# Kernel tuning notes

Measured on AMD Instinct MI355X. Metric: run time of the kernel, lower is better.

Reference implementation:

```python
import jax, jax.numpy as jnp
import numpy as np

SEQ_LEN, KEY_DIM, VAL_DIM, NUM_FEATURES, BATCH = 2048, 512, 512, 1024, 8


def setup_inputs() -> dict:
    key = jax.random.key(0)
    ks = jax.random.split(key, 7)
    x = jax.random.normal(ks[0], (BATCH, SEQ_LEN, NUM_FEATURES), dtype=jnp.float32)
    s = 1.0 / np.sqrt(NUM_FEATURES)
    Wq = jax.random.normal(ks[1], (NUM_FEATURES, KEY_DIM), dtype=jnp.float32) * s
    bq = jnp.zeros((KEY_DIM,), dtype=jnp.float32)
    Wk = jax.random.normal(ks[2], (NUM_FEATURES, KEY_DIM), dtype=jnp.float32) * s
    bk = jnp.zeros((KEY_DIM,), dtype=jnp.float32)
    Wv = jax.random.normal(ks[3], (NUM_FEATURES, VAL_DIM), dtype=jnp.float32) * s
    bv = jnp.zeros((VAL_DIM,), dtype=jnp.float32)
    return {"x": x, "Wq": Wq, "bq": bq, "Wk": Wk, "bk": bk, "Wv": Wv, "bv": bv}


def reference(x, Wq, bq, Wk, bk, Wv, bv):
    # x: [B, S, F]
    S = x.shape[1]
    q = x @ Wq + bq                      # [B, S, K]
    k = x @ Wk + bk                      # [B, S, K]
    v = x @ Wv + bv                      # [B, S, V]
    logits = jnp.einsum('bqd,bkd->bqk', q, k) / jnp.sqrt(jnp.float32(KEY_DIM))
    # additive causal mask: -inf above diagonal
    causal = jnp.tril(jnp.ones((S, S), dtype=bool))
    logits = jnp.where(causal, logits, -jnp.inf)
    probs = jax.nn.softmax(logits, axis=-1)
    read = jnp.einsum('bqk,bkv->bqv', probs, v)  # [B, S, V]
    return jnp.concatenate([x, read], axis=-1)   # [B, S, F+V]
```

## Files before the change

### kernel.cpp

```cpp
#include <hip/hip_runtime.h>

#define BB 8
#define SS 2048
#define FF 1024
#define DD 512

typedef __attribute__((ext_vector_type(4))) float f32x4;
typedef __attribute__((ext_vector_type(8))) short s16x8;
typedef __attribute__((ext_vector_type(4))) short s16x4;

__device__ __forceinline__ unsigned short f2bf(float f) {
  unsigned int u = __builtin_bit_cast(unsigned int, f);
  unsigned int r = ((u >> 16) & 1u) + 0x7fffu;
  return (unsigned short)((u + r) >> 16);
}

__device__ __forceinline__ void async16(const void* g, void* l) {
  __builtin_amdgcn_global_load_lds((const __attribute__((address_space(1))) void*)g,
                                   (__attribute__((address_space(3))) void*)l, 16, 0, 0);
}

__global__ __launch_bounds__(256) void convert_x(const float* __restrict__ x,
                                                 float* __restrict__ out,
                                                 unsigned short* __restrict__ xb) {
  size_t idx = ((size_t)blockIdx.x * 256 + threadIdx.x) * 4;
  f32x4 v = *(const f32x4*)(x + idx);
  size_t row = idx >> 10;
  size_t col = idx & 1023;
  *(f32x4*)(out + row * 1536 + col) = v;
  s16x4 h;
  h[0] = (short)f2bf(v[0]); h[1] = (short)f2bf(v[1]);
  h[2] = (short)f2bf(v[2]); h[3] = (short)f2bf(v[3]);
  *(s16x4*)(xb + idx) = h;
}

__global__ __launch_bounds__(256) void prep_w(const float* __restrict__ Wq,
                                              const float* __restrict__ Wk,
                                              const float* __restrict__ Wv,
                                              unsigned short* __restrict__ wt) {
  int z = blockIdx.z;
  const float* W = (z == 0) ? Wq : ((z == 1) ? Wk : Wv);
  unsigned short* o = wt + (size_t)z * DD * FF;
  __shared__ __align__(16) float t[32][33];
  int k0 = blockIdx.x * 32, n0 = blockIdx.y * 32;
  int tid = threadIdx.x;
  int r = tid >> 3, c4 = (tid & 7) * 4;
  f32x4 v = *(const f32x4*)(W + (size_t)(k0 + r) * DD + n0 + c4);
  t[r][c4 + 0] = v[0]; t[r][c4 + 1] = v[1]; t[r][c4 + 2] = v[2]; t[r][c4 + 3] = v[3];
  __syncthreads();
  s16x4 h;
  h[0] = (short)f2bf(t[c4 + 0][r]);
  h[1] = (short)f2bf(t[c4 + 1][r]);
  h[2] = (short)f2bf(t[c4 + 2][r]);
  h[3] = (short)f2bf(t[c4 + 3][r]);
  *(s16x4*)(o + (size_t)(n0 + r) * FF + k0 + c4) = h;
}

__global__ __launch_bounds__(256, 2) void gemm_qkv(
    const unsigned short* __restrict__ xb, const unsigned short* __restrict__ wt,
    const float* __restrict__ bq, const float* __restrict__ bk, const float* __restrict__ bv,
    unsigned short* __restrict__ qo, unsigned short* __restrict__ ko,
    unsigned short* __restrict__ vto) {
  const int wsel = blockIdx.z;
  const unsigned short* W = wt + (size_t)wsel * DD * FF;
  const float* bias = (wsel == 0) ? bq : ((wsel == 1) ? bk : bv);
  const int m0 = blockIdx.x * 128, n0 = blockIdx.y * 128;

  __shared__ __align__(16) unsigned short Al[128 * 32];
  __shared__ __align__(16) unsigned short Bl[128 * 32];

  const int tid = threadIdx.x;
  const int lane = tid & 63, wv = tid >> 6;
  const int wr = wv >> 1, wc = wv & 1;
  const int l15 = lane & 15, lg = lane >> 4;

  const f32x4 fzero = {0.f, 0.f, 0.f, 0.f};
  f32x4 acc[4][4];
#pragma unroll
  for (int i = 0; i < 4; ++i)
#pragma unroll
    for (int j = 0; j < 4; ++j) acc[i][j] = fzero;

  for (int k0 = 0; k0 < FF; k0 += 32) {
#pragma unroll
    for (int is = 0; is < 2; ++is) {
      int chunk = (is * 4 + wv) * 64;
      int lin = (chunk + lane) * 8;
      int r = lin >> 5, c = lin & 31;
      async16(xb + (size_t)(m0 + r) * FF + k0 + c, (char*)Al + (size_t)chunk * 16);
      async16(W + (size_t)(n0 + r) * FF + k0 + c, (char*)Bl + (size_t)chunk * 16);
    }
    __syncthreads();
    s16x8 af[4], bf[4];
#pragma unroll
    for (int mi = 0; mi < 4; ++mi)
      af[mi] = *(const s16x8*)(&Al[(wr * 64 + mi * 16 + l15) * 32 + lg * 8]);
#pragma unroll
    for (int ni = 0; ni < 4; ++ni)
      bf[ni] = *(const s16x8*)(&Bl[(wc * 64 + ni * 16 + l15) * 32 + lg * 8]);
#pragma unroll
    for (int mi = 0; mi < 4; ++mi)
#pragma unroll
      for (int ni = 0; ni < 4; ++ni)
        acc[mi][ni] = __builtin_amdgcn_mfma_f32_16x16x32_bf16(af[mi], bf[ni], acc[mi][ni], 0, 0, 0);
    __syncthreads();
  }

  const float QS = 0.0637583894f;
#pragma unroll
  for (int ni = 0; ni < 4; ++ni) {
    int cg = n0 + wc * 64 + ni * 16 + l15;
    float bvv = bias[cg];
#pragma unroll
    for (int mi = 0; mi < 4; ++mi) {
#pragma unroll
      for (int j = 0; j < 4; ++j) {
        int rg = m0 + wr * 64 + mi * 16 + lg * 4 + j;
        float val = acc[mi][ni][j] + bvv;
        if (wsel == 0) val *= QS;
        unsigned short h = f2bf(val);
        if (wsel == 2) {
          int bb = rg >> 11, s = rg & 2047;
          vto[((size_t)(bb * DD + cg)) * SS + s] = h;
        } else {
          unsigned short* o = wsel ? ko : qo;
          o[(size_t)rg * DD + cg] = h;
        }
      }
    }
  }
}

__global__ __launch_bounds__(256, 2) void attn(const unsigned short* __restrict__ qg,
                                               const unsigned short* __restrict__ kgl,
                                               const unsigned short* __restrict__ vtg,
                                               float* __restrict__ out) {
  const int b = blockIdx.y;
  const int vhalf = blockIdx.z;
  const int qt = (vhalf == 0) ? blockIdx.x : (31 - blockIdx.x);
  const int q0 = qt * 64;

  __shared__ __align__(16) unsigned short Kl[32 * 520];
  __shared__ __align__(16) unsigned short Vl[256 * 40];
  __shared__ __align__(16) unsigned short Pl[4 * 16 * 40];

  const int tid = threadIdx.x;
  const int lane = tid & 63, w = tid >> 6;
  const int l15 = lane & 15, lg = lane >> 4;

  s16x8 qf[16];
  {
    const unsigned short* qp = qg + ((size_t)(b * SS + q0 + w * 16 + l15)) * DD + lg * 8;
#pragma unroll
    for (int kk = 0; kk < 16; ++kk) qf[kk] = *(const s16x8*)(qp + kk * 32);
  }

  const f32x4 fzero = {0.f, 0.f, 0.f, 0.f};
  f32x4 oacc[16];
#pragma unroll
  for (int n = 0; n < 16; ++n) oacc[n] = fzero;
  float mrun[4], lrun[4];
#pragma unroll
  for (int i = 0; i < 4; ++i) { mrun[i] = -__builtin_inff(); lrun[i] = 0.f; }

  const int nt = qt * 2 + 2;
  for (int t = 0; t < nt; ++t) {
    const int kv0 = t * 32;
#pragma unroll
    for (int it = 0; it < 8; ++it) {
      int lin = (it * 256 + tid) * 8;
      int r = lin >> 9, c = lin & 511;
      *(f32x4*)(&Kl[r * 520 + c]) =
          *(const f32x4*)(kgl + ((size_t)(b * SS + kv0 + r)) * DD + c);
      if (it < 4) {
        int n = lin >> 5, c2 = lin & 31;
        *(f32x4*)(&Vl[n * 40 + c2]) =
            *(const f32x4*)(vtg + ((size_t)(b * DD + vhalf * 256 + n)) * SS + kv0 + c2);
      }
    }
    __syncthreads();

    f32x4 s0 = fzero;
    f32x4 s1 = fzero;
#pragma unroll
    for (int kk = 0; kk < 16; ++kk) {
      s16x8 b0 = *(const s16x8*)(&Kl[l15 * 520 + kk * 32 + lg * 8]);
      s16x8 b1 = *(const s16x8*)(&Kl[(16 + l15) * 520 + kk * 32 + lg * 8]);
      s0 = __builtin_amdgcn_mfma_f32_16x16x32_bf16(qf[kk], b0, s0, 0, 0, 0);
      s1 = __builtin_amdgcn_mfma_f32_16x16x32_bf16(qf[kk], b1, s1, 0, 0, 0);
    }

    const int rowb = q0 + w * 16 + lg * 4;
    if (kv0 + 31 > q0 + w * 16) {
#pragma unroll
      for (int i = 0; i < 4; ++i) {
        int rg = rowb + i;
        if (kv0 + l15 > rg)      s0[i] = -__builtin_inff();
        if (kv0 + 16 + l15 > rg) s1[i] = -__builtin_inff();
      }
    }

    float corr[4];
#pragma unroll
    for (int i = 0; i < 4; ++i) {
      float tm = fmaxf(s0[i], s1[i]);
      tm = fmaxf(tm, __shfl_xor(tm, 1));
      tm = fmaxf(tm, __shfl_xor(tm, 2));
      tm = fmaxf(tm, __shfl_xor(tm, 4));
      tm = fmaxf(tm, __shfl_xor(tm, 8));
      float mo = mrun[i];
      float mn = fmaxf(mo, tm);
      mrun[i] = mn;
      float mne = fmaxf(mn, -1e30f);
      float c = __builtin_amdgcn_exp2f(fmaxf(mo, -1e30f) - mne);
      float p0 = __builtin_amdgcn_exp2f(s0[i] - mne);
      float p1 = __builtin_amdgcn_exp2f(s1[i] - mne);
      float rs = p0 + p1;
      rs += __shfl_xor(rs, 1);
      rs += __shfl_xor(rs, 2);
      rs += __shfl_xor(rs, 4);
      rs += __shfl_xor(rs, 8);
      lrun[i] = lrun[i] * c + rs;
      corr[i] = c;
      Pl[w * 640 + (lg * 4 + i) * 40 + l15] = f2bf(p0);
      Pl[w * 640 + (lg * 4 + i) * 40 + 16 + l15] = f2bf(p1);
    }

#pragma unroll
    for (int n = 0; n < 16; ++n) {
      oacc[n][0] *= corr[0]; oacc[n][1] *= corr[1];
      oacc[n][2] *= corr[2]; oacc[n][3] *= corr[3];
    }

    asm volatile("s_waitcnt lgkmcnt(0)" ::: "memory");
    s16x8 pa = *(const s16x8*)(&Pl[w * 640 + l15 * 40 + lg * 8]);
#pragma unroll
    for (int n = 0; n < 16; ++n) {
      s16x8 vb = *(const s16x8*)(&Vl[(n * 16 + l15) * 40 + lg * 8]);
      oacc[n] = __builtin_amdgcn_mfma_f32_16x16x32_bf16(pa, vb, oacc[n], 0, 0, 0);
    }
    __syncthreads();
  }

  float inv[4];
#pragma unroll
  for (int i = 0; i < 4; ++i) inv[i] = 1.0f / lrun[i];
  size_t obase = ((size_t)(b * SS + q0 + w * 16 + lg * 4)) * 1536 + 1024 + vhalf * 256;
#pragma unroll
  for (int n = 0; n < 16; ++n) {
#pragma unroll
    for (int i = 0; i < 4; ++i) {
      out[obase + (size_t)i * 1536 + n * 16 + l15] = oacc[n][i] * inv[i];
    }
  }
}

extern "C" void kernel_launch(void* const* d_in, const int* in_sizes, int n_in,
                              void* d_out, int out_size, void* d_ws, size_t ws_size,
                              hipStream_t stream) {
  (void)in_sizes; (void)n_in; (void)out_size; (void)ws_size;
  const float* x  = (const float*)d_in[0];
  const float* Wq = (const float*)d_in[1];
  const float* bq = (const float*)d_in[2];
  const float* Wk = (const float*)d_in[3];
  const float* bk = (const float*)d_in[4];
  const float* Wv = (const float*)d_in[5];
  const float* bv = (const float*)d_in[6];
  float* out = (float*)d_out;

  char* ws = (char*)d_ws;
  unsigned short* xb  = (unsigned short*)(ws);
  unsigned short* wt  = (unsigned short*)(ws + 33554432);
  unsigned short* qw  = (unsigned short*)(ws + 33554432 + 3145728);
  unsigned short* kw  = qw + (size_t)16384 * 512;
  unsigned short* vtw = kw + (size_t)16384 * 512;

  convert_x<<<16384, 256, 0, stream>>>(x, out, xb);
  prep_w<<<dim3(32, 16, 3), 256, 0, stream>>>(Wq, Wk, Wv, wt);
  gemm_qkv<<<dim3(128, 4, 3), 256, 0, stream>>>(xb, wt, bq, bk, bv, qw, kw, vtw);
  attn<<<dim3(32, 8, 2), 256, 0, stream>>>(qw, kw, vtw, out);
}
```

Before: 434.1 us.

## Use single-wave attention blocks reading K/V from global and stage V-transpose via LDS

The attention kernel is rewritten so that each 64-thread block handles 16 query rows. It loads K and V fragments directly from global memory (relying on L2/cache) instead of staging them in shared memory with block-wide barriers, and it drops the -1e30 clamping in the softmax. The grid grows to 128x8x2 with longest tiles first, to improve load balance across the causal triangle and remove syncthreads. Separately, the QKV GEMM epilogue for V now transposes through LDS and writes 16-byte vectors instead of scattered 2-byte stores. The trade-off is that K and V are no longer shared across waves in a block, so global/L2 traffic rises.

```diff
diff --git a/kernel.cpp b/kernel.cpp
--- a/kernel.cpp
+++ b/kernel.cpp
@@ -66,8 +66,9 @@
   const float* bias = (wsel == 0) ? bq : ((wsel == 1) ? bk : bv);
   const int m0 = blockIdx.x * 128, n0 = blockIdx.y * 128;
 
-  __shared__ __align__(16) unsigned short Al[128 * 32];
-  __shared__ __align__(16) unsigned short Bl[128 * 32];
+  __shared__ __align__(16) char smem[36864];
+  unsigned short* Al = (unsigned short*)smem;
+  unsigned short* Bl = (unsigned short*)(smem + 8192);
 
   const int tid = threadIdx.x;
   const int lane = tid & 63, wv = tid >> 6;
@@ -107,50 +108,66 @@
   }
 
   const float QS = 0.0637583894f;
-#pragma unroll
-  for (int ni = 0; ni < 4; ++ni) {
-    int cg = n0 + wc * 64 + ni * 16 + l15;
-    float bvv = bias[cg];
-#pragma unroll
-    for (int mi = 0; mi < 4; ++mi) {
-#pragma unroll
-      for (int j = 0; j < 4; ++j) {
-        int rg = m0 + wr * 64 + mi * 16 + lg * 4 + j;
-        float val = acc[mi][ni][j] + bvv;
-        if (wsel == 0) val *= QS;
-        unsigned short h = f2bf(val);
-        if (wsel == 2) {
-          int bb = rg >> 11, s = rg & 2047;
-          vto[((size_t)(bb * DD + cg)) * SS + s] = h;
-        } else {
-          unsigned short* o = wsel ? ko : qo;
-          o[(size_t)rg * DD + cg] = h;
+  if (wsel == 2) {
+    unsigned short* Tw = (unsigned short*)smem + (size_t)wv * 64 * 72;
+#pragma unroll
+    for (int ni = 0; ni < 4; ++ni) {
+      int cl = ni * 16 + l15;
+      float bvv = bias[n0 + wc * 64 + cl];
+#pragma unroll
+      for (int mi = 0; mi < 4; ++mi)
+#pragma unroll
+        for (int j = 0; j < 4; ++j)
+          Tw[cl * 72 + mi * 16 + lg * 4 + j] = f2bf(acc[mi][ni][j] + bvv);
+    }
+    asm volatile("s_waitcnt lgkmcnt(0)" ::: "memory");
+    const int bb = (m0 + wr * 64) >> 11;
+    const int sb = (m0 + wr * 64) & 2047;
+    const int cb = n0 + wc * 64;
+#pragma unroll
+    for (int p = 0; p < 8; ++p) {
+      int cl = p * 8 + (lane >> 3);
+      int sl = (lane & 7) * 8;
+      s16x8 vv = *(const s16x8*)(Tw + cl * 72 + sl);
+      *(s16x8*)(vto + ((size_t)(bb * DD + cb + cl)) * SS + sb + sl) = vv;
+    }
+  } else {
+    unsigned short* o = wsel ? ko : qo;
+#pragma unroll
+    for (int ni = 0; ni < 4; ++ni) {
+      int cg = n0 + wc * 64 + ni * 16 + l15;
+      float bvv = bias[cg];
+#pragma unroll
+      for (int mi = 0; mi < 4; ++mi) {
+#pragma unroll
+        for (int j = 0; j < 4; ++j) {
+          int rg = m0 + wr * 64 + mi * 16 + lg * 4 + j;
+          float val = acc[mi][ni][j] + bvv;
+          if (wsel == 0) val *= QS;
+          o[(size_t)rg * DD + cg] = f2bf(val);
         }
       }
     }
   }
 }
 
-__global__ __launch_bounds__(256, 2) void attn(const unsigned short* __restrict__ qg,
-                                               const unsigned short* __restrict__ kgl,
-                                               const unsigned short* __restrict__ vtg,
-                                               float* __restrict__ out) {
+__global__ __launch_bounds__(64) void attn(const unsigned short* __restrict__ qg,
+                                           const unsigned short* __restrict__ kgl,
+                                           const unsigned short* __restrict__ vtg,
+                                           float* __restrict__ out) {
+  const int r16 = 127 - (int)blockIdx.x;
   const int b = blockIdx.y;
   const int vhalf = blockIdx.z;
-  const int qt = (vhalf == 0) ? blockIdx.x : (31 - blockIdx.x);
-  const int q0 = qt * 64;
-
-  __shared__ __align__(16) unsigned short Kl[32 * 520];
-  __shared__ __align__(16) unsigned short Vl[256 * 40];
-  __shared__ __align__(16) unsigned short Pl[4 * 16 * 40];
-
-  const int tid = threadIdx.x;
-  const int lane = tid & 63, w = tid >> 6;
+  const int rowb0 = r16 * 16;
+
+  __shared__ __align__(16) unsigned short Pl[16 * 40];
+
+  const int lane = threadIdx.x & 63;
   const int l15 = lane & 15, lg = lane >> 4;
 
   s16x8 qf[16];
   {
-    const unsigned short* qp = qg + ((size_t)(b * SS + q0 + w * 16 + l15)) * DD + lg * 8;
+    const unsigned short* qp = qg + ((size_t)(b * SS + rowb0 + l15)) * DD + lg * 8;
 #pragma unroll
     for (int kk = 0; kk < 16; ++kk) qf[kk] = *(const s16x8*)(qp + kk * 32);
   }
@@ -163,38 +180,27 @@
 #pragma unroll
   for (int i = 0; i < 4; ++i) { mrun[i] = -__builtin_inff(); lrun[i] = 0.f; }
 
-  const int nt = qt * 2 + 2;
+  const unsigned short* kb = kgl + (size_t)b * SS * DD;
+  const unsigned short* vb0 = vtg + ((size_t)(b * DD + vhalf * 256)) * SS;
+
+  const int nt = (r16 >> 1) + 1;
   for (int t = 0; t < nt; ++t) {
     const int kv0 = t * 32;
-#pragma unroll
-    for (int it = 0; it < 8; ++it) {
-      int lin = (it * 256 + tid) * 8;
-      int r = lin >> 9, c = lin & 511;
-      *(f32x4*)(&Kl[r * 520 + c]) =
-          *(const f32x4*)(kgl + ((size_t)(b * SS + kv0 + r)) * DD + c);
-      if (it < 4) {
-        int n = lin >> 5, c2 = lin & 31;
-        *(f32x4*)(&Vl[n * 40 + c2]) =
-            *(const f32x4*)(vtg + ((size_t)(b * DD + vhalf * 256 + n)) * SS + kv0 + c2);
-      }
-    }
-    __syncthreads();
-
-    f32x4 s0 = fzero;
-    f32x4 s1 = fzero;
+
+    f32x4 s0 = fzero, s1 = fzero;
+    const unsigned short* kp = kb + (size_t)(kv0 + l15) * DD + lg * 8;
 #pragma unroll
     for (int kk = 0; kk < 16; ++kk) {
-      s16x8 b0 = *(const s16x8*)(&Kl[l15 * 520 + kk * 32 + lg * 8]);
-      s16x8 b1 = *(const s16x8*)(&Kl[(16 + l15) * 520 + kk * 32 + lg * 8]);
+      s16x8 b0 = *(const s16x8*)(kp + kk * 32);
+      s16x8 b1 = *(const s16x8*)(kp + 16 * DD + kk * 32);
       s0 = __builtin_amdgcn_mfma_f32_16x16x32_bf16(qf[kk], b0, s0, 0, 0, 0);
       s1 = __builtin_amdgcn_mfma_f32_16x16x32_bf16(qf[kk], b1, s1, 0, 0, 0);
     }
 
-    const int rowb = q0 + w * 16 + lg * 4;
-    if (kv0 + 31 > q0 + w * 16) {
+    if (kv0 + 31 > rowb0) {
 #pragma unroll
       for (int i = 0; i < 4; ++i) {
-        int rg = rowb + i;
+        int rg = rowb0 + lg * 4 + i;
         if (kv0 + l15 > rg)      s0[i] = -__builtin_inff();
         if (kv0 + 16 + l15 > rg) s1[i] = -__builtin_inff();
       }
@@ -211,10 +217,9 @@
       float mo = mrun[i];
       float mn = fmaxf(mo, tm);
       mrun[i] = mn;
-      float mne = fmaxf(mn, -1e30f);
-      float c = __builtin_amdgcn_exp2f(fmaxf(mo, -1e30f) - mne);
-      float p0 = __builtin_amdgcn_exp2f(s0[i] - mne);
-      float p1 = __builtin_amdgcn_exp2f(s1[i] - mne);
+      float c = __builtin_amdgcn_exp2f(mo - mn);
+      float p0 = __builtin_amdgcn_exp2f(s0[i] - mn);
+      float p1 = __builtin_amdgcn_exp2f(s1[i] - mn);
       float rs = p0 + p1;
       rs += __shfl_xor(rs, 1);
       rs += __shfl_xor(rs, 2);
@@ -222,8 +227,8 @@
       rs += __shfl_xor(rs, 8);
       lrun[i] = lrun[i] * c + rs;
       corr[i] = c;
-      Pl[w * 640 + (lg * 4 + i) * 40 + l15] = f2bf(p0);
-      Pl[w * 640 + (lg * 4 + i) * 40 + 16 + l15] = f2bf(p1);
+      Pl[(lg * 4 + i) * 40 + l15] = f2bf(p0);
+      Pl[(lg * 4 + i) * 40 + 16 + l15] = f2bf(p1);
     }
 
 #pragma unroll
@@ -233,19 +238,18 @@
     }
 
     asm volatile("s_waitcnt lgkmcnt(0)" ::: "memory");
-    s16x8 pa = *(const s16x8*)(&Pl[w * 640 + l15 * 40 + lg * 8]);
+    s16x8 pa = *(const s16x8*)(&Pl[l15 * 40 + lg * 8]);
 #pragma unroll
     for (int n = 0; n < 16; ++n) {
-      s16x8 vb = *(const s16x8*)(&Vl[(n * 16 + l15) * 40 + lg * 8]);
-      oacc[n] = __builtin_amdgcn_mfma_f32_16x16x32_bf16(pa, vb, oacc[n], 0, 0, 0);
-    }
-    __syncthreads();
+      s16x8 vv = *(const s16x8*)(vb0 + (size_t)(n * 16 + l15) * SS + kv0 + lg * 8);
+      oacc[n] = __builtin_amdgcn_mfma_f32_16x16x32_bf16(pa, vv, oacc[n], 0, 0, 0);
+    }
   }
 
   float inv[4];
 #pragma unroll
   for (int i = 0; i < 4; ++i) inv[i] = 1.0f / lrun[i];
-  size_t obase = ((size_t)(b * SS + q0 + w * 16 + lg * 4)) * 1536 + 1024 + vhalf * 256;
+  size_t obase = ((size_t)(b * SS + rowb0 + lg * 4)) * 1536 + 1024 + vhalf * 256;
 #pragma unroll
   for (int n = 0; n < 16; ++n) {
 #pragma unroll
@@ -278,5 +282,5 @@
   convert_x<<<16384, 256, 0, stream>>>(x, out, xb);
   prep_w<<<dim3(32, 16, 3), 256, 0, stream>>>(Wq, Wk, Wv, wt);
   gemm_qkv<<<dim3(128, 4, 3), 256, 0, stream>>>(xb, wt, bq, bk, bv, qw, kw, vtw);
-  attn<<<dim3(32, 8, 2), 256, 0, stream>>>(qw, kw, vtw, out);
-}
+  attn<<<dim3(128, 8, 2), 64, 0, stream>>>(qw, kw, vtw, out);
+}
```

After: 1.012 ms. +133.0%, slower.
